# Optimization experiments

Hardware: AMD Instinct MI355X
Metric: run time of the kernel (lower is better)

The kernel has to match this reference:

```python
import jax, jax.numpy as jnp
import numpy as np

B = 512        # batch
S = 256        # grid side; P = S*S input pixels/nodes
P = S * S
NOUT = 512     # number of regions (output nodes of FGL)
COUT = 4       # FGL output channels
NCLS = 10      # classifier classes


def setup_inputs() -> dict:
    key = jax.random.key(0)
    k1, k2, k3, k4 = jax.random.split(key, 4)
    x = jax.random.normal(k1, (B, P), dtype=jnp.float32)
    # region assignment per pixel (edge-list form of variable-length adj lists)
    seg_ids = jax.random.randint(k2, (P,), 0, NOUT)
    W_fgl = jax.random.normal(k3, (COUT, NOUT), dtype=jnp.float32) * 0.05
    b_fgl = jnp.zeros((COUT, NOUT), dtype=jnp.float32)
    W_fc = jax.random.normal(k4, (NOUT * COUT, NCLS), dtype=jnp.float32) * 0.02
    b_fc = jnp.zeros((NCLS,), dtype=jnp.float32)
    return {"x": x, "W_fgl": W_fgl, "b_fgl": b_fgl, "W_fc": W_fc,
            "b_fc": b_fc, "seg_ids": seg_ids}


def reference(x, W_fgl, b_fgl, W_fc, b_fc, seg_ids):
    # FGL, op_order '213': (2) sum-reduce pixels into regions via adjacency,
    # (1) per-region channel weight (cin=1 -> cout), (3) bias.
    # h[j, n] = sum_{p: seg[p]==j} x[n, p]
    h = jax.ops.segment_sum(x.T, seg_ids, num_segments=NOUT)  # [NOUT, B]
    h = h.T                                                   # [B, NOUT]
    y = h[:, None, :] * W_fgl[None, :, :] + b_fgl[None, :, :]  # [B, COUT, NOUT]
    y = y.reshape(x.shape[0], -1)                             # [B, COUT*NOUT]
    return y @ W_fc + b_fc                                    # [B, NCLS]
```

## Files before the change

kernel.cpp:

```cpp
#include <hip/hip_runtime.h>

#define BATCH 512
#define PIX   65536
#define NOUT  512
#define COUT  4
#define NCLS  10

#define KC    2048
#define NKC   (PIX / KC)
#define NRG   (BATCH / 8)
#define AWROW 4112

typedef __fp16 half2_t __attribute__((ext_vector_type(2)));

#if __has_builtin(__builtin_amdgcn_fdot2)
__device__ __forceinline__ float fdot2f(half2_t a, half2_t b, float c) {
    return __builtin_amdgcn_fdot2(a, b, c, false);
}
#else
__device__ __forceinline__ float fdot2f(half2_t a, half2_t b, float c) {
    return c + (float)a[0] * (float)b[0] + (float)a[1] * (float)b[1];
}
#endif

__global__ __launch_bounds__(512) void weff_kernel(
    const float* __restrict__ W_fgl, const float* __restrict__ b_fgl,
    const float* __restrict__ W_fc,  const float* __restrict__ b_fc,
    unsigned* __restrict__ Weff_h, float* __restrict__ out)
{
    const int j = threadIdx.x;

    float wf[COUT], bf[COUT];
#pragma unroll
    for (int c = 0; c < COUT; ++c) {
        wf[c] = W_fgl[c * NOUT + j];
        bf[c] = b_fgl[c * NOUT + j];
    }

    float wv[NCLS], cpart[NCLS];
#pragma unroll
    for (int k = 0; k < NCLS; ++k) {
        float w = 0.f, cb = 0.f;
#pragma unroll
        for (int c = 0; c < COUT; ++c) {
            const float wfc = W_fc[(c * NOUT + j) * NCLS + k];
            w  += wf[c] * wfc;
            cb += bf[c] * wfc;
        }
        wv[k]    = w;
        cpart[k] = cb;
    }

#pragma unroll
    for (int k5 = 0; k5 < 5; ++k5) {
        const half2_t h = __builtin_amdgcn_cvt_pkrtz(wv[2 * k5], wv[2 * k5 + 1]);
        Weff_h[j * 5 + k5] = __builtin_bit_cast(unsigned, h);
    }

#pragma unroll
    for (int k = 0; k < NCLS; ++k)
#pragma unroll
        for (int off = 32; off; off >>= 1)
            cpart[k] += __shfl_down(cpart[k], off);

    __shared__ float red[8 * NCLS];
    __shared__ float cs[NCLS];
    if ((j & 63) == 0) {
#pragma unroll
        for (int k = 0; k < NCLS; ++k) red[(j >> 6) * NCLS + k] = cpart[k];
    }
    __syncthreads();
    if (j < NCLS) {
        float s = b_fc[j];
#pragma unroll
        for (int w = 0; w < 8; ++w) s += red[w * NCLS + j];
        cs[j] = s;
    }
    __syncthreads();
    for (int i = j; i < BATCH * NCLS; i += 512) out[i] = cs[i % NCLS];
}

__global__ __launch_bounds__(256) void awbuild_kernel(
    const int* __restrict__ seg, const unsigned* __restrict__ Weff_h,
    unsigned short* __restrict__ AwT)
{
    const int p = blockIdx.x * 256 + threadIdx.x;
    const int j = seg[p];
    const unsigned* wrow = Weff_h + j * 5;
#pragma unroll
    for (int k5 = 0; k5 < 5; ++k5) {
        const unsigned u = wrow[k5];
        AwT[(size_t)(2 * k5)     * PIX + p] = (unsigned short)(u & 0xffffu);
        AwT[(size_t)(2 * k5 + 1) * PIX + p] = (unsigned short)(u >> 16);
    }
}

__global__ __launch_bounds__(256) void gemm_kernel(
    const float* __restrict__ x, const unsigned short* __restrict__ AwT,
    float* __restrict__ out)
{
    __shared__ __align__(16) char smem[10 * AWROW];
    const int t    = threadIdx.x;
    const int rowg = blockIdx.x & (NRG - 1);
    const int kc   = blockIdx.x >> 6;
    const int pc   = kc * KC;

#pragma unroll
    for (int k = 0; k < NCLS; ++k) {
        const uint4 v = *(const uint4*)(AwT + (size_t)k * PIX + pc + t * 8);
        *(uint4*)(smem + k * AWROW + t * 16) = v;
    }
    __syncthreads();

    const int w = t >> 6, lane = t & 63;
    const int r0 = rowg * 8 + w * 2;
    const float4* __restrict__ xa = (const float4*)(x + (size_t)r0 * PIX + pc);
    const float4* __restrict__ xb = (const float4*)(x + (size_t)(r0 + 1) * PIX + pc);

    float acc0[NCLS] = {}, acc1[NCLS] = {};
#pragma unroll 2
    for (int i = 0; i < KC / 4 / 64; ++i) {
        const int px4 = i * 64 + lane;
        const float4 va = xa[px4];
        const float4 vb = xb[px4];
        uint2 awv[NCLS];
#pragma unroll
        for (int k = 0; k < NCLS; ++k)
            awv[k] = *(const uint2*)(smem + k * AWROW + px4 * 8);
        const half2_t a0 = __builtin_amdgcn_cvt_pkrtz(va.x, va.y);
        const half2_t a1 = __builtin_amdgcn_cvt_pkrtz(va.z, va.w);
        const half2_t b0 = __builtin_amdgcn_cvt_pkrtz(vb.x, vb.y);
        const half2_t b1 = __builtin_amdgcn_cvt_pkrtz(vb.z, vb.w);
#pragma unroll
        for (int k = 0; k < NCLS; ++k) {
            const half2_t wlo = __builtin_bit_cast(half2_t, awv[k].x);
            const half2_t whi = __builtin_bit_cast(half2_t, awv[k].y);
            acc0[k] = fdot2f(a1, whi, fdot2f(a0, wlo, acc0[k]));
            acc1[k] = fdot2f(b1, whi, fdot2f(b0, wlo, acc1[k]));
        }
    }
    __syncthreads();

    float* part = (float*)smem;
#pragma unroll
    for (int k = 0; k < NCLS; ++k) {
        part[k * 264 + t]          = acc0[k];
        part[(10 + k) * 264 + t]   = acc1[k];
    }
    __syncthreads();

    if (t < 80) {
        const int w2 = t / 20, j = t % 20;
        const float4* src = (const float4*)(part + j * 264 + w2 * 64);
        float4 s4 = src[0];
#pragma unroll
        for (int q = 1; q < 16; ++q) {
            const float4 v = src[q];
            s4.x += v.x; s4.y += v.y; s4.z += v.z; s4.w += v.w;
        }
        const float s = (s4.x + s4.y) + (s4.z + s4.w);
        const int r = j / 10, k = j % 10;
        unsafeAtomicAdd(&out[(rowg * 8 + w2 * 2 + r) * NCLS + k], s);
    }
}

extern "C" void kernel_launch(void* const* d_in, const int* in_sizes, int n_in,
                              void* d_out, int out_size, void* d_ws, size_t ws_size,
                              hipStream_t stream)
{
    const float* x     = (const float*)d_in[0];
    const float* W_fgl = (const float*)d_in[1];
    const float* b_fgl = (const float*)d_in[2];
    const float* W_fc  = (const float*)d_in[3];
    const float* b_fc  = (const float*)d_in[4];
    const int*   seg   = (const int*)d_in[5];
    float*       out   = (float*)d_out;

    char*           ws     = (char*)d_ws;
    unsigned*       Weff_h = (unsigned*)ws;
    unsigned short* AwT    = (unsigned short*)(ws + 16384);

    weff_kernel   <<<dim3(1),          512, 0, stream>>>(W_fgl, b_fgl, W_fc, b_fc,
                                                         Weff_h, out);
    awbuild_kernel<<<dim3(PIX / 256),  256, 0, stream>>>(seg, Weff_h, AwT);
    gemm_kernel   <<<dim3(NRG * NKC),  256, 0, stream>>>(x, AwT, out);
}
```

Measured before the change: 35.08 us.

## Fuse weight folding and AwT build into the GEMM kernel

Every GEMM block now recomputes the folded per-region half-precision weights in shared memory and builds its own AwT chunk from seg ids, so the separate weff and awbuild kernels and the AwT round trip through global memory go away. The bias constant is added by the kc==0 blocks, and the output is zeroed with a memset. The cost is that all 2048 blocks repeat the weight folding (reading W_fc, about 80KB each, mostly from L2), and shared memory use per block grows.

```diff
diff --git a/kernel.cpp b/kernel.cpp
--- a/kernel.cpp
+++ b/kernel.cpp
@@ -23,38 +23,53 @@
 }
 #endif
 
-__global__ __launch_bounds__(512) void weff_kernel(
+__global__ __launch_bounds__(256) void fused_gemm_kernel(
+    const float* __restrict__ x, const int* __restrict__ seg,
     const float* __restrict__ W_fgl, const float* __restrict__ b_fgl,
     const float* __restrict__ W_fc,  const float* __restrict__ b_fc,
-    unsigned* __restrict__ Weff_h, float* __restrict__ out)
+    float* __restrict__ out)
 {
-    const int j = threadIdx.x;
+    __shared__ unsigned wh[NOUT * 5];
+    __shared__ __align__(16) char awmem[10 * AWROW];
+    __shared__ float red[4 * NCLS];
+    __shared__ float cs[NCLS];
 
-    float wf[COUT], bf[COUT];
+    const int t    = threadIdx.x;
+    const int rowg = blockIdx.x & (NRG - 1);
+    const int kc   = blockIdx.x >> 6;
+    const int pc   = kc * KC;
+
+    float cpart[NCLS];
 #pragma unroll
-    for (int c = 0; c < COUT; ++c) {
-        wf[c] = W_fgl[c * NOUT + j];
-        bf[c] = b_fgl[c * NOUT + j];
-    }
+    for (int k = 0; k < NCLS; ++k) cpart[k] = 0.f;
 
-    float wv[NCLS], cpart[NCLS];
 #pragma unroll
-    for (int k = 0; k < NCLS; ++k) {
-        float w = 0.f, cb = 0.f;
+    for (int jj = 0; jj < 2; ++jj) {
+        const int j = jj * 256 + t;
+        float wf[COUT], bf[COUT];
 #pragma unroll
         for (int c = 0; c < COUT; ++c) {
-            const float wfc = W_fc[(c * NOUT + j) * NCLS + k];
-            w  += wf[c] * wfc;
-            cb += bf[c] * wfc;
+            wf[c] = W_fgl[c * NOUT + j];
+            bf[c] = b_fgl[c * NOUT + j];
         }
-        wv[k]    = w;
-        cpart[k] = cb;
-    }
-
+        float wv[NCLS];
 #pragma unroll
-    for (int k5 = 0; k5 < 5; ++k5) {
-        const half2_t h = __builtin_amdgcn_cvt_pkrtz(wv[2 * k5], wv[2 * k5 + 1]);
-        Weff_h[j * 5 + k5] = __builtin_bit_cast(unsigned, h);
+        for (int k = 0; k < NCLS; ++k) {
+            float w = 0.f, cb = 0.f;
+#pragma unroll
+            for (int c = 0; c < COUT; ++c) {
+                const float wfc = W_fc[(c * NOUT + j) * NCLS + k];
+                w  += wf[c] * wfc;
+                cb += bf[c] * wfc;
+            }
+            wv[k] = w;
+            cpart[k] += cb;
+        }
+#pragma unroll
+        for (int k5 = 0; k5 < 5; ++k5) {
+            const half2_t h = __builtin_amdgcn_cvt_pkrtz(wv[2 * k5], wv[2 * k5 + 1]);
+            wh[j * 5 + k5] = __builtin_bit_cast(unsigned, h);
+        }
     }
 
 #pragma unroll
@@ -62,53 +77,32 @@
 #pragma unroll
         for (int off = 32; off; off >>= 1)
             cpart[k] += __shfl_down(cpart[k], off);
-
-    __shared__ float red[8 * NCLS];
-    __shared__ float cs[NCLS];
-    if ((j & 63) == 0) {
+    if ((t & 63) == 0) {
 #pragma unroll
-        for (int k = 0; k < NCLS; ++k) red[(j >> 6) * NCLS + k] = cpart[k];
+        for (int k = 0; k < NCLS; ++k) red[(t >> 6) * NCLS + k] = cpart[k];
     }
     __syncthreads();
-    if (j < NCLS) {
-        float s = b_fc[j];
+    if (t < NCLS) {
+        float s = b_fc[t];
 #pragma unroll
-        for (int w = 0; w < 8; ++w) s += red[w * NCLS + j];
-        cs[j] = s;
+        for (int w2 = 0; w2 < 4; ++w2) s += red[w2 * NCLS + t];
+        cs[t] = s;
     }
-    __syncthreads();
-    for (int i = j; i < BATCH * NCLS; i += 512) out[i] = cs[i % NCLS];
-}
-
-__global__ __launch_bounds__(256) void awbuild_kernel(
-    const int* __restrict__ seg, const unsigned* __restrict__ Weff_h,
-    unsigned short* __restrict__ AwT)
-{
-    const int p = blockIdx.x * 256 + threadIdx.x;
-    const int j = seg[p];
-    const unsigned* wrow = Weff_h + j * 5;
-#pragma unroll
-    for (int k5 = 0; k5 < 5; ++k5) {
-        const unsigned u = wrow[k5];
-        AwT[(size_t)(2 * k5)     * PIX + p] = (unsigned short)(u & 0xffffu);
-        AwT[(size_t)(2 * k5 + 1) * PIX + p] = (unsigned short)(u >> 16);
-    }
-}
-
-__global__ __launch_bounds__(256) void gemm_kernel(
-    const float* __restrict__ x, const unsigned short* __restrict__ AwT,
-    float* __restrict__ out)
-{
-    __shared__ __align__(16) char smem[10 * AWROW];
-    const int t    = threadIdx.x;
-    const int rowg = blockIdx.x & (NRG - 1);
-    const int kc   = blockIdx.x >> 6;
-    const int pc   = kc * KC;
 
 #pragma unroll
-    for (int k = 0; k < NCLS; ++k) {
-        const uint4 v = *(const uint4*)(AwT + (size_t)k * PIX + pc + t * 8);
-        *(uint4*)(smem + k * AWROW + t * 16) = v;
+    for (int i = 0; i < 4; ++i) {
+        const int pr = i * 256 + t;
+        const int2 js = *(const int2*)(seg + pc + pr * 2);
+        const unsigned* wa = &wh[js.x * 5];
+        const unsigned* wb = &wh[js.y * 5];
+#pragma unroll
+        for (int k5 = 0; k5 < 5; ++k5) {
+            const unsigned a = wa[k5], b = wb[k5];
+            *(unsigned*)(awmem + (2 * k5)     * AWROW + pr * 4) =
+                (a & 0xffffu) | (b << 16);
+            *(unsigned*)(awmem + (2 * k5 + 1) * AWROW + pr * 4) =
+                (a >> 16) | (b & 0xffff0000u);
+        }
     }
     __syncthreads();
 
@@ -126,7 +120,7 @@
         uint2 awv[NCLS];
 #pragma unroll
         for (int k = 0; k < NCLS; ++k)
-            awv[k] = *(const uint2*)(smem + k * AWROW + px4 * 8);
+            awv[k] = *(const uint2*)(awmem + k * AWROW + px4 * 8);
         const half2_t a0 = __builtin_amdgcn_cvt_pkrtz(va.x, va.y);
         const half2_t a1 = __builtin_amdgcn_cvt_pkrtz(va.z, va.w);
         const half2_t b0 = __builtin_amdgcn_cvt_pkrtz(vb.x, vb.y);
@@ -141,11 +135,11 @@
     }
     __syncthreads();
 
-    float* part = (float*)smem;
+    float* part = (float*)awmem;
 #pragma unroll
     for (int k = 0; k < NCLS; ++k) {
-        part[k * 264 + t]          = acc0[k];
-        part[(10 + k) * 264 + t]   = acc1[k];
+        part[k * 264 + t]        = acc0[k];
+        part[(10 + k) * 264 + t] = acc1[k];
     }
     __syncthreads();
 
@@ -158,8 +152,9 @@
             const float4 v = src[q];
             s4.x += v.x; s4.y += v.y; s4.z += v.z; s4.w += v.w;
         }
-        const float s = (s4.x + s4.y) + (s4.z + s4.w);
         const int r = j / 10, k = j % 10;
+        float s = (s4.x + s4.y) + (s4.z + s4.w);
+        if (kc == 0) s += cs[k];
         unsafeAtomicAdd(&out[(rowg * 8 + w2 * 2 + r) * NCLS + k], s);
     }
 }
@@ -176,12 +171,8 @@
     const int*   seg   = (const int*)d_in[5];
     float*       out   = (float*)d_out;
 
-    char*           ws     = (char*)d_ws;
-    unsigned*       Weff_h = (unsigned*)ws;
-    unsigned short* AwT    = (unsigned short*)(ws + 16384);
+    hipMemsetAsync(out, 0, (size_t)BATCH * NCLS * sizeof(float), stream);
 
-    weff_kernel   <<<dim3(1),          512, 0, stream>>>(W_fgl, b_fgl, W_fc, b_fc,
-                                                         Weff_h, out);
-    awbuild_kernel<<<dim3(PIX / 256),  256, 0, stream>>>(seg, Weff_h, AwT);
-    gemm_kernel   <<<dim3(NRG * NKC),  256, 0, stream>>>(x, AwT, out);
+    fused_gemm_kernel<<<dim3(NRG * NKC), 256, 0, stream>>>(
+        x, seg, W_fgl, b_fgl, W_fc, b_fc, out);
 }
```

Measured after the change: 43.60 us. 24.3% more time.
